# Optimization experiments

Hardware: AMD Instinct MI355X
Metric: run time of the kernel (lower is better)

## Reference

```python
import jax, jax.numpy as jnp
import numpy as np

B, L, D, H, DH, MAX_SEQ = 2, 2048, 512, 8, 64, 2048


def setup_inputs() -> dict:
    key = jax.random.key(0)
    ks = jax.random.split(key, 9)
    w = 0.02
    return {
        "q": jax.random.normal(ks[0], (B, L, D), jnp.float32),
        "k": jax.random.normal(ks[1], (B, L, D), jnp.float32),
        "v": jax.random.normal(ks[2], (B, L, D), jnp.float32),
        "Wq_w": jax.random.normal(ks[3], (D, D), jnp.float32) * w,
        "Wq_b": jnp.zeros((D,), jnp.float32),
        "Wk_w": jax.random.normal(ks[4], (D, D), jnp.float32) * w,
        "Wk_b": jnp.zeros((D,), jnp.float32),
        "Wv_w": jax.random.normal(ks[5], (D, D), jnp.float32) * w,
        "Wv_b": jnp.zeros((D,), jnp.float32),
        "fc_w": jax.random.normal(ks[6], (D, D), jnp.float32) * w,
        "fc_b": jnp.zeros((D,), jnp.float32),
        "E": jax.random.normal(ks[7], (MAX_SEQ, DH), jnp.float32),
        "mask": jnp.triu(jnp.ones((L, L), jnp.int32), k=1)[None, None],  # 1 = masked
    }


def reference(q, k, v, Wq_w, Wq_b, Wk_w, Wk_b, Wv_w, Wv_b, fc_w, fc_b, E, mask):
    b, lq, d = q.shape

    def proj(x, w, bias):
        # torch Linear: x @ W.T + b, then split heads -> [b, h, l, dh]
        y = x @ w.T + bias
        return y.reshape(b, -1, H, DH).transpose(0, 2, 1, 3)

    qh, kh, vh = proj(q, Wq_w, Wq_b), proj(k, Wk_w, Wk_b), proj(v, Wv_w, Wv_b)
    len_q, len_k = qh.shape[2], kh.shape[2]

    # relative embedding slice (starting_point = max(0, max_seq - len_q))
    e = E[max(0, MAX_SEQ - len_q):, :]          # [m, dh], m == len_q here
    m = e.shape[0]

    QE = jnp.einsum('bhld,md->bhlm', qh, e)      # [b,h,lq,m]
    # qe_masking: keep column j of row i iff j >= m-1-i
    keep = (jnp.arange(m)[None, :] >= (m - 1 - jnp.arange(len_q))[:, None])
    QE = QE * keep.astype(QE.dtype)

    # skewing: left-pad last dim, reshape swapping trailing dims, drop first row
    padded = jnp.pad(QE, ((0, 0), (0, 0), (0, 0), (1, 0)))      # [b,h,lq,m+1]
    Srel = padded.reshape(b, H, m + 1, len_q)[:, :, 1:, :]       # [b,h,m,lq]
    if len_k > len_q:
        Srel = jnp.pad(Srel, ((0, 0), (0, 0), (0, len_k - len_q), (0, 0)))
    elif len_k < len_q:
        Srel = Srel[:, :, :, :len_k]

    QKt = jnp.einsum('bhld,bhmd->bhlm', qh, kh)                  # [b,h,lq,lk]
    logits = (QKt + Srel) / jnp.sqrt(jnp.float32(DH))
    logits = logits + mask.astype(logits.dtype) * jnp.float32(-1e9)
    attn = jax.nn.softmax(logits, axis=-1)
    out = jnp.einsum('bhlm,bhmd->bhld', attn, vh)                # [b,h,lq,dh]
    out = out.transpose(0, 2, 1, 3).reshape(b, len_q, d)
    out = out @ fc_w.T + fc_b
    return out, attn
```

## Files before the change

kernel.cpp:

```cpp
#include <hip/hip_runtime.h>
#include <hip/hip_bf16.h>
#include <cstdint>

typedef __bf16 bf16;
typedef __attribute__((ext_vector_type(8))) __bf16 bf16x8;
typedef __attribute__((ext_vector_type(4))) __bf16 bf16x4;
typedef __attribute__((ext_vector_type(4))) float f32x4;

#define MFMA16 __builtin_amdgcn_mfma_f32_16x16x32_bf16
#define MASKV (-1e30f)

static constexpr int Lq  = 2048;
static constexpr int BKt = 64;

__device__ __forceinline__ void async_load16(const void* g, void* l) {
  __builtin_amdgcn_global_load_lds(
      (__attribute__((address_space(1))) void*)g,
      (__attribute__((address_space(3))) void*)l, 16, 0, 0);
}

__global__ void convert_all(const float* __restrict__ q, const float* __restrict__ k,
                            const float* __restrict__ v, const float* __restrict__ wq,
                            const float* __restrict__ wk, const float* __restrict__ wv,
                            const float* __restrict__ fc, const float* __restrict__ E,
                            bf16* q_bf, bf16* k_bf, bf16* v_bf, bf16* wq_bf,
                            bf16* wk_bf, bf16* wv_bf, bf16* fc_bf, bf16* E_bf,
                            float* s_buf)
{
  int i = blockIdx.x * blockDim.x + threadIdx.x;
  const float* src; bf16* dst; int rel;
  if      (i < 524288)  { src = q;  dst = q_bf;  rel = i; }
  else if (i < 1048576) { src = k;  dst = k_bf;  rel = i - 524288; }
  else if (i < 1572864) { src = v;  dst = v_bf;  rel = i - 1048576; }
  else if (i < 1638400) { src = wq; dst = wq_bf; rel = i - 1572864; }
  else if (i < 1703936) { src = wk; dst = wk_bf; rel = i - 1638400; }
  else if (i < 1769472) { src = wv; dst = wv_bf; rel = i - 1703936; }
  else if (i < 1835008) { src = fc; dst = fc_bf; rel = i - 1769472; }
  else if (i < 1867776) { src = E;  dst = E_bf;  rel = i - 1835008; }
  else if (i < 1875968) {
    ((float4*)s_buf)[i - 1867776] = make_float4(0.f, 0.f, 0.f, 0.f);
    return;
  }
  else return;
  float4 x = *(const float4*)(src + (size_t)rel * 4);
  bf16x4 o;
  o[0] = (bf16)x.x; o[1] = (bf16)x.y; o[2] = (bf16)x.z; o[3] = (bf16)x.w;
  *(bf16x4*)(dst + (size_t)rel * 4) = o;
}

template<int MODE>
__device__ __forceinline__
void gemm512_core(const bf16* __restrict__ A, const bf16* __restrict__ Bm,
                  const float* __restrict__ bias, void* __restrict__ Cv,
                  int tm, int tn, char* lA, char* lB)
{
  const int tid = threadIdx.x, lane = tid & 63, wv = tid >> 6;
  const int wr = wv >> 1, wc = wv & 1;

  f32x4 acc[4][4];
#pragma unroll
  for (int m = 0; m < 4; ++m)
#pragma unroll
    for (int n = 0; n < 4; ++n) acc[m][n] = (f32x4){0.f, 0.f, 0.f, 0.f};

  for (int k0 = 0; k0 < 512; k0 += 64) {
    __syncthreads();
#pragma unroll
    for (int it = 0; it < 4; ++it) {
      int slot = it * 256 + wv * 64 + lane;
      int row = slot >> 3, c = slot & 7;
      int gk = k0 + ((c ^ (row & 7)) * 8);
      async_load16(A  + (size_t)(tm * 128 + row) * 512 + gk, lA + (it * 256 + wv * 64) * 16);
      async_load16(Bm + (size_t)(tn * 128 + row) * 512 + gk, lB + (it * 256 + wv * 64) * 16);
    }
    __syncthreads();
#pragma unroll
    for (int kc = 0; kc < 2; ++kc) {
      bf16x8 af[4], bfr[4];
#pragma unroll
      for (int m = 0; m < 4; ++m) {
        int row = wr * 64 + m * 16 + (lane & 15);
        int ch = ((lane >> 4) + kc * 4) ^ (row & 7);
        af[m] = *(const bf16x8*)(lA + row * 128 + ch * 16);
      }
#pragma unroll
      for (int n = 0; n < 4; ++n) {
        int row = wc * 64 + n * 16 + (lane & 15);
        int ch = ((lane >> 4) + kc * 4) ^ (row & 7);
        bfr[n] = *(const bf16x8*)(lB + row * 128 + ch * 16);
      }
#pragma unroll
      for (int m = 0; m < 4; ++m)
#pragma unroll
        for (int n = 0; n < 4; ++n)
          acc[m][n] = MFMA16(af[m], bfr[n], acc[m][n], 0, 0, 0);
    }
  }

#pragma unroll
  for (int m = 0; m < 4; ++m)
#pragma unroll
    for (int n = 0; n < 4; ++n)
#pragma unroll
      for (int r = 0; r < 4; ++r) {
        int gi = tm * 128 + wr * 64 + m * 16 + 4 * (lane >> 4) + r;
        int gj = tn * 128 + wc * 64 + n * 16 + (lane & 15);
        float vv = acc[m][n][r] + ((MODE == 2) ? bias[gi] : bias[gj]);
        if (MODE == 3) {
          ((float*)Cv)[(size_t)gi * 512 + gj] = vv;
        } else if (MODE == 2) {
          int h = gi >> 6, dh = gi & 63, b = gj >> 11, l = gj & 2047;
          ((bf16*)Cv)[((size_t)((b * 8 + h) * 64 + dh)) * 2048 + l] = (bf16)vv;
        } else {
          int b = gi >> 11, l = gi & 2047, h = gj >> 6, dh = gj & 63;
          ((bf16*)Cv)[((size_t)((b * 8 + h) * 2048 + l)) * 64 + dh] = (bf16)vv;
        }
      }
}

__global__ __launch_bounds__(256, 2)
void gemm_qkv(const bf16* __restrict__ q_bf, const bf16* __restrict__ k_bf,
              const bf16* __restrict__ v_bf, const bf16* __restrict__ wq_bf,
              const bf16* __restrict__ wk_bf, const bf16* __restrict__ wv_bf,
              const float* __restrict__ wq_b, const float* __restrict__ wk_b,
              const float* __restrict__ wv_b,
              bf16* __restrict__ qh, bf16* __restrict__ kh, bf16* __restrict__ vt)
{
  __shared__ __align__(16) char lA[16384];
  __shared__ __align__(16) char lB[16384];
  const int z = blockIdx.z;
  if (z == 0)      gemm512_core<0>(q_bf, wq_bf, wq_b, qh, blockIdx.x, blockIdx.y, lA, lB);
  else if (z == 1) gemm512_core<0>(k_bf, wk_bf, wk_b, kh, blockIdx.x, blockIdx.y, lA, lB);
  else             gemm512_core<2>(wv_bf, v_bf, wv_b, vt, blockIdx.y, blockIdx.x, lA, lB);
}

__global__ __launch_bounds__(256, 2)
void gemm_fc(const bf16* __restrict__ A, const bf16* __restrict__ Bm,
             const float* __restrict__ bias, float* __restrict__ Cv)
{
  __shared__ __align__(16) char lA[16384];
  __shared__ __align__(16) char lB[16384];
  gemm512_core<3>(A, Bm, bias, Cv, blockIdx.x, blockIdx.y, lA, lB);
}

__device__ __forceinline__ void stage_k(const bf16* __restrict__ kb, int j0,
                                        char* dst, int tid) {
#pragma unroll
  for (int it = 0; it < 2; ++it) {
    int slot = it * 256 + tid;
    int row = slot >> 3, c = slot & 7;
    async_load16(kb + (size_t)(j0 + row) * 64 + ((c ^ (row & 7)) * 8), dst + slot * 16);
  }
}
__device__ __forceinline__ void stage_v(const bf16* __restrict__ vb, int j0,
                                        char* dst, int tid) {
#pragma unroll
  for (int it = 0; it < 2; ++it) {
    int slot = it * 256 + tid;
    int row = slot >> 3, c = slot & 7;
    async_load16(vb + (size_t)row * Lq + j0 + ((c ^ (row & 7)) * 8), dst + slot * 16);
  }
}

__device__ __forceinline__ void attn_logits_sh(
    int i0, int j0, int wvx, int lane,
    const bf16x8 qf0, const bf16x8 qf1,
    const bf16* __restrict__ Ebf, const char* lk, f32x4 acc_s[4])
{
  const int rbase = i0 + wvx * 16 - j0 - 63;
  f32x4 acc_t[5];
#pragma unroll
  for (int cf = 0; cf < 5; ++cf) {
    int r = rbase + cf * 16 + (lane & 15);
    int re = 2047 - r; re = re < 0 ? 0 : (re > 2047 ? 2047 : re);
    const bf16* ep = Ebf + (size_t)re * 64 + (lane >> 4) * 8;
    f32x4 a = (f32x4){0.f, 0.f, 0.f, 0.f};
    a = MFMA16(qf0, *(const bf16x8*)ep, a, 0, 0, 0);
    a = MFMA16(qf1, *(const bf16x8*)(ep + 32), a, 0, 0, 0);
    acc_t[cf] = a;
  }
#pragma unroll
  for (int cf = 0; cf < 4; ++cf) {
    int key = cf * 16 + (lane & 15);
    int c0 = (lane >> 4) ^ (key & 7);
    int c1 = ((lane >> 4) + 4) ^ (key & 7);
    f32x4 a = (f32x4){0.f, 0.f, 0.f, 0.f};
    a = MFMA16(qf0, *(const bf16x8*)(lk + key * 128 + c0 * 16), a, 0, 0, 0);
    a = MFMA16(qf1, *(const bf16x8*)(lk + key * 128 + c1 * 16), a, 0, 0, 0);
    acc_s[cf] = a;
  }
  const int g = lane >> 4, b = lane & 15;
#pragma unroll
  for (int r = 0; r < 4; ++r) {
    const int qw  = 4 * g + r;
    const int sl  = (lane & 48) | ((63 + qw - b) & 15);
    const bool hi = qw > b;
#pragma unroll
    for (int cf = 0; cf < 4; ++cf) {
      float vhi = __shfl(acc_t[4 - cf][r], sl);
      float vlo = __shfl(acc_t[3 - cf][r], sl);
      float t = hi ? vhi : vlo;
      float vv = (acc_s[cf][r] + t) * 0.125f;
      if (j0 + cf * 16 + b > i0 + wvx * 16 + qw) vv = MASKV;
      acc_s[cf][r] = vv;
    }
  }
}

__global__ __launch_bounds__(256, 4)
void produce(const bf16* __restrict__ qh, const bf16* __restrict__ kh,
             const bf16* __restrict__ vt, const bf16* __restrict__ Ebf,
             bf16* __restrict__ P_scr, float* __restrict__ O_slots,
             float* __restrict__ s_buf, float* __restrict__ attn_out)
{
  __shared__ __align__(16) char lds_k[2][64 * 128];
  __shared__ __align__(16) char lds_v[2][64 * 128];
  __shared__ __align__(16) char lds_p[4][16 * 64 * 2];

  const int tid = threadIdx.x, lane = tid & 63, wvx = tid >> 6;
  const int n    = blockIdx.x;
  const int xcd  = n & 7;
  const int r0   = n >> 3;
  const int bh   = 2 * xcd + (r0 & 1);
  const int u    = r0 >> 1;
  const int f    = u & 7;
  const int qt   = 31 - (u >> 3);
  const int nc   = (qt >> 2) + 1;
  if (f >= nc) return;
  const int i0   = qt * 64;
  const int jbeg = f * 4;
  const int jend = (jbeg + 4 < qt + 1) ? jbeg + 4 : qt + 1;

  const bf16* qb = qh + (size_t)bh * Lq * 64;
  const bf16* kb = kh + (size_t)bh * Lq * 64;
  const bf16* vb = vt + (size_t)bh * 64 * Lq;
  float* attn_b = attn_out + (size_t)bh * Lq * Lq;
  bf16* P_b = P_scr + (size_t)bh * Lq * Lq;
  bf16* pst = (bf16*)lds_p[wvx];

  const int qrow = i0 + wvx * 16 + (lane & 15);
  const bf16x8 qf0 = *(const bf16x8*)(qb + (size_t)qrow * 64 + (lane >> 4) * 8);
  const bf16x8 qf1 = *(const bf16x8*)(qb + (size_t)qrow * 64 + 32 + (lane >> 4) * 8);

  f32x4 acc_s[4];
  f32x4 acc_o[4];
  float s_acc[4] = {0.f, 0.f, 0.f, 0.f};
#pragma unroll
  for (int nn = 0; nn < 4; ++nn) acc_o[nn] = (f32x4){0.f, 0.f, 0.f, 0.f};

  stage_k(kb, jbeg * BKt, lds_k[0], tid);
  stage_v(vb, jbeg * BKt, lds_v[0], tid);
  asm volatile("s_waitcnt vmcnt(0)" ::: "memory");
  __builtin_amdgcn_s_barrier();

  int lt = 0;
  for (int jt = jbeg; jt < jend; ++jt) {
    const int j0 = jt * BKt;
    const bool pre = (jt + 1 < jend);
    attn_logits_sh(i0, j0, wvx, lane, qf0, qf1, Ebf, lds_k[lt], acc_s);
    if (pre) {
      stage_k(kb, j0 + BKt, lds_k[lt ^ 1], tid);
      stage_v(vb, j0 + BKt, lds_v[lt ^ 1], tid);
    }
#pragma unroll
    for (int cf = 0; cf < 4; ++cf) {
      int kl = cf * 16 + (lane & 15);
      int chs = kl >> 3;
#pragma unroll
      for (int r = 0; r < 4; ++r) {
        int qw = 4 * (lane >> 4) + r;
        float p = __expf(acc_s[cf][r]);
        s_acc[r] += p;
        pst[qw * 64 + ((chs ^ (qw & 7)) * 8) + (kl & 7)] = (bf16)p;
      }
    }
    asm volatile("s_waitcnt lgkmcnt(0)" ::: "memory");
    __builtin_amdgcn_sched_barrier(0);
#pragma unroll
    for (int it = 0; it < 2; ++it) {
      int qw = it * 8 + (lane >> 3);
      int c = lane & 7;
      bf16x8 pv = *(const bf16x8*)(pst + qw * 64 + ((c ^ (qw & 7)) * 8));
      *(bf16x8*)(P_b + (size_t)(i0 + wvx * 16 + qw) * Lq + j0 + c * 8) = pv;
    }
    __builtin_amdgcn_s_setprio(1);
#pragma unroll
    for (int kc = 0; kc < 2; ++kc) {
      int qa = lane & 15;
      int cha = (kc * 4 + (lane >> 4)) ^ (qa & 7);
      bf16x8 pf = *(const bf16x8*)(pst + qa * 64 + cha * 8);
#pragma unroll
      for (int nn = 0; nn < 4; ++nn) {
        int dh = nn * 16 + (lane & 15);
        int chv = (kc * 4 + (lane >> 4)) ^ (dh & 7);
        bf16x8 vf = *(const bf16x8*)(lds_v[lt] + dh * 128 + chv * 16);
        acc_o[nn] = MFMA16(pf, vf, acc_o[nn], 0, 0, 0);
      }
    }
    __builtin_amdgcn_s_setprio(0);
    if (pre) {
      asm volatile("s_waitcnt vmcnt(2)" ::: "memory");
      __builtin_amdgcn_s_barrier();
      lt ^= 1;
    }
  }

  float* oslot = O_slots + (size_t)(((bh * 32 + qt) * 8 + f)) * 4096;
#pragma unroll
  for (int nn = 0; nn < 4; ++nn)
#pragma unroll
    for (int r = 0; r < 4; ++r) {
      int row = wvx * 16 + 4 * (lane >> 4) + r;
      oslot[row * 64 + nn * 16 + (lane & 15)] = acc_o[nn][r];
    }

#pragma unroll
  for (int r = 0; r < 4; ++r) {
    float s = s_acc[r];
    for (int d = 1; d < 16; d <<= 1) s += __shfl_xor(s, d);
    if ((lane & 15) == 0)
      atomicAdd(&s_buf[bh * Lq + i0 + wvx * 16 + 4 * (lane >> 4) + r], s);
  }

  for (int jz = qt + 1 + f; jz < 32; jz += nc) {
    const int j0 = jz * BKt;
#pragma unroll
    for (int kk = 0; kk < 4; ++kk) {
      int idx = kk * 256 + tid;
      int row = idx >> 4, c4 = idx & 15;
      float* p = attn_b + (size_t)(i0 + row) * Lq + j0 + c4 * 4;
      *(float4*)p = make_float4(0.f, 0.f, 0.f, 0.f);
    }
  }
}

__global__ __launch_bounds__(256, 8)
void finish(const bf16* __restrict__ P_scr, const float* __restrict__ s_buf,
            float* __restrict__ attn_out)
{
  const int lane = threadIdx.x & 63, wvx = threadIdx.x >> 6;
  const int row = blockIdx.x * 4 + wvx;
  const int i   = row & 2047;
  const int ncols = (i & ~63) + 64;
  const float inv = 1.f / s_buf[row];
  const bf16* src = P_scr + (size_t)row * Lq;
  float* dst = attn_out + (size_t)row * Lq;
  for (int c = lane * 4; c < ncols; c += 256) {
    bf16x4 pv = *(const bf16x4*)(src + c);
    float4 fo;
    fo.x = (float)pv[0] * inv;
    fo.y = (float)pv[1] * inv;
    fo.z = (float)pv[2] * inv;
    fo.w = (float)pv[3] * inv;
    *(float4*)(dst + c) = fo;
  }
}

__global__ void combine_o(const float* __restrict__ O_slots,
                          const float* __restrict__ s_buf, bf16* __restrict__ oh)
{
  const int sid = blockIdx.x;
  const int bh = sid >> 5, qt = sid & 31;
  const int nch = (qt >> 2) + 1;
  const float* base = O_slots + (size_t)(bh * 32 + qt) * 8 * 4096;
  const int b = bh >> 3, h = bh & 7;
  for (int e4 = threadIdx.x; e4 < 1024; e4 += 256) {
    float4 s = make_float4(0.f, 0.f, 0.f, 0.f);
    for (int ff = 0; ff < nch; ++ff) {
      float4 x = *(const float4*)(base + ff * 4096 + e4 * 4);
      s.x += x.x; s.y += x.y; s.z += x.z; s.w += x.w;
    }
    int row = e4 >> 4;
    int col = (e4 & 15) * 4;
    int ig = qt * 64 + row;
    float inv = 1.f / s_buf[bh * Lq + ig];
    bf16x4 o;
    o[0] = (bf16)(s.x * inv); o[1] = (bf16)(s.y * inv);
    o[2] = (bf16)(s.z * inv); o[3] = (bf16)(s.w * inv);
    *(bf16x4*)(oh + (size_t)(b * 2048 + ig) * 512 + h * 64 + col) = o;
  }
}

extern "C" void kernel_launch(void* const* d_in, const int* in_sizes, int n_in,
                              void* d_out, int out_size, void* d_ws, size_t ws_size,
                              hipStream_t stream) {
  const float* q    = (const float*)d_in[0];
  const float* k    = (const float*)d_in[1];
  const float* v    = (const float*)d_in[2];
  const float* wq   = (const float*)d_in[3];
  const float* wq_b = (const float*)d_in[4];
  const float* wk   = (const float*)d_in[5];
  const float* wk_b = (const float*)d_in[6];
  const float* wv   = (const float*)d_in[7];
  const float* wv_b = (const float*)d_in[8];
  const float* fc   = (const float*)d_in[9];
  const float* fc_b = (const float*)d_in[10];
  const float* E    = (const float*)d_in[11];

  if (ws_size < 233177088) return;
  char* ws = (char*)d_ws;
  bf16*  q_bf    = (bf16*)(ws);
  bf16*  k_bf    = (bf16*)(ws + 4194304);
  bf16*  v_bf    = (bf16*)(ws + 8388608);
  bf16*  wq_bf   = (bf16*)(ws + 12582912);
  bf16*  wk_bf   = (bf16*)(ws + 13107200);
  bf16*  wv_bf   = (bf16*)(ws + 13631488);
  bf16*  fc_bf   = (bf16*)(ws + 14155776);
  bf16*  E_bf    = (bf16*)(ws + 14680064);
  float* s_buf   = (float*)(ws + 14942208);
  bf16*  qh_bf   = (bf16*)(ws + 15073280);
  bf16*  kh_bf   = (bf16*)(ws + 19267584);
  bf16*  vt_bf   = (bf16*)(ws + 23461888);
  bf16*  oh_bf   = (bf16*)(ws + 27656192);
  float* O_slots = (float*)(ws + 31850496);
  bf16*  P_scr   = (bf16*)(ws + 98959360);

  float* out_f  = (float*)d_out;
  float* attn_f = out_f + 2097152;

  convert_all<<<7328, 256, 0, stream>>>(q, k, v, wq, wk, wv, fc, E,
      q_bf, k_bf, v_bf, wq_bf, wk_bf, wv_bf, fc_bf, E_bf, s_buf);
  gemm_qkv<<<dim3(32, 4, 3), 256, 0, stream>>>(q_bf, k_bf, v_bf,
      wq_bf, wk_bf, wv_bf, wq_b, wk_b, wv_b, qh_bf, kh_bf, vt_bf);
  produce<<<4096, 256, 0, stream>>>(qh_bf, kh_bf, vt_bf, E_bf,
                                    P_scr, O_slots, s_buf, attn_f);
  finish<<<8192, 256, 0, stream>>>(P_scr, s_buf, attn_f);
  combine_o<<<512, 256, 0, stream>>>(O_slots, s_buf, oh_bf);
  gemm_fc<<<dim3(32, 4), 256, 0, stream>>>(oh_bf, fc_bf, fc_b, out_f);
}
```

Baseline: 196.0 us.

## Compact produce grid, move attn zero-fill into finish, pack skew shuffles to bf16

The produce launch now enumerates only valid (query tile, chunk) pairs through a small loop, so no blocks are launched just to exit early. Zero-filling of the causal-masked attention region moves from produce into finish, which now writes every column of each row with contiguous stores. The relative-embedding skew exchange packs two bf16 values per shuffle, halving cross-lane shuffles at the cost of rounding that term to bf16.

Result: slower. 204.3 us (+4.2%).

```diff
diff --git a/kernel.cpp b/kernel.cpp
--- a/kernel.cpp
+++ b/kernel.cpp
@@ -17,6 +17,14 @@
   __builtin_amdgcn_global_load_lds(
       (__attribute__((address_space(1))) void*)g,
       (__attribute__((address_space(3))) void*)l, 16, 0, 0);
+}
+
+__device__ __forceinline__ unsigned pack2bf(float lo, float hi) {
+  bf16 a = (bf16)lo, c = (bf16)hi;
+  unsigned short ua, uc;
+  __builtin_memcpy(&ua, &a, 2);
+  __builtin_memcpy(&uc, &c, 2);
+  return ((unsigned)uc << 16) | ua;
 }
 
 __global__ void convert_all(const float* __restrict__ q, const float* __restrict__ k,
@@ -189,6 +197,13 @@
     a = MFMA16(qf1, *(const bf16x8*)(lk + key * 128 + c1 * 16), a, 0, 0, 0);
     acc_s[cf] = a;
   }
+  unsigned pr[4][4];
+#pragma unroll
+  for (int c = 0; c < 4; ++c)
+#pragma unroll
+    for (int r = 0; r < 4; ++r)
+      pr[c][r] = pack2bf(acc_t[c][r], acc_t[c + 1][r]);
+
   const int g = lane >> 4, b = lane & 15;
 #pragma unroll
   for (int r = 0; r < 4; ++r) {
@@ -197,9 +212,9 @@
     const bool hi = qw > b;
 #pragma unroll
     for (int cf = 0; cf < 4; ++cf) {
-      float vhi = __shfl(acc_t[4 - cf][r], sl);
-      float vlo = __shfl(acc_t[3 - cf][r], sl);
-      float t = hi ? vhi : vlo;
+      unsigned u = __shfl(pr[3 - cf][r], sl);
+      float t = hi ? __uint_as_float(u & 0xffff0000u)
+                   : __uint_as_float(u << 16);
       float vv = (acc_s[cf][r] + t) * 0.125f;
       if (j0 + cf * 16 + b > i0 + wvx * 16 + qw) vv = MASKV;
       acc_s[cf][r] = vv;
@@ -211,22 +226,24 @@
 void produce(const bf16* __restrict__ qh, const bf16* __restrict__ kh,
              const bf16* __restrict__ vt, const bf16* __restrict__ Ebf,
              bf16* __restrict__ P_scr, float* __restrict__ O_slots,
-             float* __restrict__ s_buf, float* __restrict__ attn_out)
+             float* __restrict__ s_buf)
 {
   __shared__ __align__(16) char lds_k[2][64 * 128];
   __shared__ __align__(16) char lds_v[2][64 * 128];
   __shared__ __align__(16) char lds_p[4][16 * 64 * 2];
 
   const int tid = threadIdx.x, lane = tid & 63, wvx = tid >> 6;
-  const int n    = blockIdx.x;
-  const int xcd  = n & 7;
-  const int r0   = n >> 3;
-  const int bh   = 2 * xcd + (r0 & 1);
-  const int u    = r0 >> 1;
-  const int f    = u & 7;
-  const int qt   = 31 - (u >> 3);
-  const int nc   = (qt >> 2) + 1;
-  if (f >= nc) return;
+  const int n   = blockIdx.x;
+  const int xcd = n & 7;
+  const int m   = n >> 3;
+  const int bh  = 2 * xcd + (m & 1);
+  int rem = m >> 1, qt = 31, f = 0;
+#pragma unroll 1
+  for (int q = 31; q >= 0; --q) {
+    int c = (q >> 2) + 1;
+    if (rem < c) { qt = q; f = rem; break; }
+    rem -= c;
+  }
   const int i0   = qt * 64;
   const int jbeg = f * 4;
   const int jend = (jbeg + 4 < qt + 1) ? jbeg + 4 : qt + 1;
@@ -234,7 +251,6 @@
   const bf16* qb = qh + (size_t)bh * Lq * 64;
   const bf16* kb = kh + (size_t)bh * Lq * 64;
   const bf16* vb = vt + (size_t)bh * 64 * Lq;
-  float* attn_b = attn_out + (size_t)bh * Lq * Lq;
   bf16* P_b = P_scr + (size_t)bh * Lq * Lq;
   bf16* pst = (bf16*)lds_p[wvx];
 
@@ -321,17 +337,6 @@
     if ((lane & 15) == 0)
       atomicAdd(&s_buf[bh * Lq + i0 + wvx * 16 + 4 * (lane >> 4) + r], s);
   }
-
-  for (int jz = qt + 1 + f; jz < 32; jz += nc) {
-    const int j0 = jz * BKt;
-#pragma unroll
-    for (int kk = 0; kk < 4; ++kk) {
-      int idx = kk * 256 + tid;
-      int row = idx >> 4, c4 = idx & 15;
-      float* p = attn_b + (size_t)(i0 + row) * Lq + j0 + c4 * 4;
-      *(float4*)p = make_float4(0.f, 0.f, 0.f, 0.f);
-    }
-  }
 }
 
 __global__ __launch_bounds__(256, 8)
@@ -345,13 +350,19 @@
   const float inv = 1.f / s_buf[row];
   const bf16* src = P_scr + (size_t)row * Lq;
   float* dst = attn_out + (size_t)row * Lq;
-  for (int c = lane * 4; c < ncols; c += 256) {
-    bf16x4 pv = *(const bf16x4*)(src + c);
+#pragma unroll
+  for (int c0 = 0; c0 < 2048; c0 += 256) {
+    const int c = c0 + lane * 4;
     float4 fo;
-    fo.x = (float)pv[0] * inv;
-    fo.y = (float)pv[1] * inv;
-    fo.z = (float)pv[2] * inv;
-    fo.w = (float)pv[3] * inv;
+    if (c < ncols) {
+      bf16x4 pv = *(const bf16x4*)(src + c);
+      fo.x = (float)pv[0] * inv;
+      fo.y = (float)pv[1] * inv;
+      fo.z = (float)pv[2] * inv;
+      fo.w = (float)pv[3] * inv;
+    } else {
+      fo = make_float4(0.f, 0.f, 0.f, 0.f);
+    }
     *(float4*)(dst + c) = fo;
   }
 }
@@ -422,8 +433,8 @@
       q_bf, k_bf, v_bf, wq_bf, wk_bf, wv_bf, fc_bf, E_bf, s_buf);
   gemm_qkv<<<dim3(32, 4, 3), 256, 0, stream>>>(q_bf, k_bf, v_bf,
       wq_bf, wk_bf, wv_bf, wq_b, wk_b, wv_b, qh_bf, kh_bf, vt_bf);
-  produce<<<4096, 256, 0, stream>>>(qh_bf, kh_bf, vt_bf, E_bf,
-                                    P_scr, O_slots, s_buf, attn_f);
+  produce<<<2304, 256, 0, stream>>>(qh_bf, kh_bf, vt_bf, E_bf,
+                                    P_scr, O_slots, s_buf);
   finish<<<8192, 256, 0, stream>>>(P_scr, s_buf, attn_f);
   combine_o<<<512, 256, 0, stream>>>(O_slots, s_buf, oh_bf);
   gemm_fc<<<dim3(32, 4), 256, 0, stream>>>(oh_bf, fc_bf, fc_b, out_f);
```
